# Kernel optimization log

Measured on AMD Instinct MI355X. Metric: run time of the kernel, lower is better.

Reference implementation:

```python
import jax, jax.numpy as jnp
import numpy as np

B, S, E, H, D = 4, 2048, 1024, 8, 128
EPS = 1e-5


def _ln(x, g, b):
    m = jnp.mean(x, axis=-1, keepdims=True)
    v = jnp.mean((x - m) ** 2, axis=-1, keepdims=True)
    return (x - m) * jax.lax.rsqrt(v + EPS) * g + b


def _xavier(k, shape, fan_in, fan_out):
    lim = float(np.sqrt(6.0 / (fan_in + fan_out)))
    return jax.random.uniform(k, shape, jnp.float32, -lim, lim)


def setup_inputs() -> dict:
    key = jax.random.key(0)
    ks = jax.random.split(key, 10)
    return {
        "x": jax.random.normal(ks[0], (B, S, E), jnp.float32),
        # embedding_to_z: Linear(E, H*D); stored as [E, H*D] for x @ W
        "W_ez": _xavier(ks[1], (E, H * D), E, H * D),
        "b_ez": jnp.zeros((H * D,), jnp.float32),
        "U_h": _xavier(ks[2], (H, D, D), D, D),
        "U_z": _xavier(ks[3], (H, D, D), D, D),
        "b_u": jnp.zeros((H, D), jnp.float32),
        "out_shaper": _xavier(ks[4], (H, D, D), D, D),
        # shared per-step state LayerNorm
        "lns_g": jnp.ones((D,), jnp.float32),
        "lns_b": jnp.zeros((D,), jnp.float32),
        # per-head FFN: LayerNorm(D) -> Linear(D,D) -> GELU -> Linear(D,E)
        "ff_ln_g": jnp.ones((H, D), jnp.float32),
        "ff_ln_b": jnp.zeros((H, D), jnp.float32),
        "ff_W1": _xavier(ks[5], (H, D, D), D, D),
        "ff_b1": jnp.zeros((H, D), jnp.float32),
        "ff_W2": _xavier(ks[6], (H, D, E), D, E),
        "ff_b2": jnp.zeros((H, E), jnp.float32),
        # layer_attention_weights: Linear(E, 1)
        "w_att": _xavier(ks[7], (E,), E, 1),
        "b_att": jnp.zeros((), jnp.float32),
        # output LayerNorm
        "lno_g": jnp.ones((E,), jnp.float32),
        "lno_b": jnp.zeros((E,), jnp.float32),
    }


def reference(x, W_ez, b_ez, U_h, U_z, b_u, out_shaper, lns_g, lns_b,
              ff_ln_g, ff_ln_b, ff_W1, ff_b1, ff_W2, ff_b2,
              w_att, b_att, lno_g, lno_b):
    b, s, _ = x.shape
    h, d = U_h.shape[0], U_h.shape[1]
    # z tokens: [B,S,H,D]
    z = jnp.tanh((x @ W_ez + b_ez).reshape(b, s, h, d))
    # torch.einsum('bhd,hdd->bhd') takes the DIAGONAL of the second operand
    uh_diag = jnp.einsum('hii->hi', U_h)          # [H,D]
    uz_diag = jnp.einsum('hii->hi', U_z)          # [H,D]
    os_diag = jnp.einsum('hii->hi', out_shaper)   # [H,D]

    def step(h_prev, z_t):
        # h_prev, z_t: [B,H,D]
        u = jax.nn.sigmoid(h_prev * uh_diag + z_t * uz_diag + b_u)
        h_new = u * h_prev + (1.0 - u) * z_t
        h_new = _ln(h_new, lns_g, lns_b)
        return h_new, h_new

    h0 = jnp.zeros((b, h, d), x.dtype)
    _, states = jax.lax.scan(step, h0, jnp.swapaxes(z, 0, 1))  # [S,B,H,D]
    states = jnp.swapaxes(states, 0, 1)                         # [B,S,H,D]

    shaped = states * os_diag                                   # diag einsum
    hln = _ln(shaped, ff_ln_g, ff_ln_b)                         # per-head LN
    h1 = jax.nn.gelu(jnp.einsum('bshd,hde->bshe', hln, ff_W1) + ff_b1,
                     approximate=False)                         # [B,S,H,D]
    ff_out = jnp.einsum('bshd,hde->bshe', h1, ff_W2) + ff_b2    # [B,S,H,E]

    scores = jax.nn.softmax(jnp.einsum('bshe,e->bsh', ff_out, w_att) + b_att,
                            axis=2)                             # over heads
    weighted = jnp.einsum('bshe,bsh->bse', ff_out, scores)      # [B,S,E]
    return _ln(weighted, lno_g, lno_b)
```

## Files before the change

kernel.cpp:

```cpp
#include <hip/hip_runtime.h>
#include <hip/hip_bf16.h>
#include <math.h>

#define BB 4
#define SS 2048
#define EE 1024
#define HH 8
#define DD 128
#define BSR (BB*SS)
#define HD  (HH*DD)
#define LNEPS 1e-5f
#define LOG2E 1.4426950408889634f

typedef __attribute__((ext_vector_type(8))) short bf16x8;
typedef __attribute__((ext_vector_type(4))) float f32x4;

__device__ __forceinline__ ushort f2bf(float f) {
    union { float f; unsigned u; } c{f};
    unsigned r = c.u + 0x7fff + ((c.u >> 16) & 1);
    return (ushort)(r >> 16);
}
__device__ __forceinline__ float bf2f(ushort b) {
    union { unsigned u; float f; } c{(unsigned)b << 16};
    return c.f;
}

typedef __attribute__((address_space(1))) const unsigned int GUI;
typedef __attribute__((address_space(3))) unsigned int LUI;
__device__ __forceinline__ void gl_lds16(const ushort* g, ushort* l) {
    __builtin_amdgcn_global_load_lds((GUI*)g, (LUI*)l, 16, 0, 0);
}

__global__ __launch_bounds__(256)
void prep_k(const float* __restrict__ W2, const float* __restrict__ w_att,
            const float* __restrict__ b2, const float* __restrict__ b_att,
            const float* __restrict__ Uh, const float* __restrict__ Uz,
            const float* __restrict__ Os,
            float* __restrict__ q, float* __restrict__ c,
            float* __restrict__ uh_d, float* __restrict__ uz_d,
            float* __restrict__ os_d)
{
    const int gid  = blockIdx.x * 256 + threadIdx.x;
    const int wave = gid >> 6, lane = gid & 63;
    if (wave < HD) {
        const float* wp = W2 + (size_t)wave * EE;
        float p = 0.f;
        for (int e = lane; e < EE; e += 64) p = fmaf(wp[e], w_att[e], p);
        #pragma unroll
        for (int off = 32; off > 0; off >>= 1) p += __shfl_xor(p, off, 64);
        if (lane == 0) {
            q[wave] = p;
            const int h = wave >> 7, d = wave & 127;
            uh_d[wave] = Uh[(size_t)h*DD*DD + (size_t)d*DD + d];
            uz_d[wave] = Uz[(size_t)h*DD*DD + (size_t)d*DD + d];
            os_d[wave] = Os[(size_t)h*DD*DD + (size_t)d*DD + d];
        }
    } else if (wave < HD + HH) {
        const int h = wave - HD;
        const float* bp = b2 + (size_t)h * EE;
        float p = 0.f;
        for (int e = lane; e < EE; e += 64) p = fmaf(bp[e], w_att[e], p);
        #pragma unroll
        for (int off = 32; off > 0; off >>= 1) p += __shfl_xor(p, off, 64);
        if (lane == 0) c[h] = p + b_att[0];
    }
}

__global__ __launch_bounds__(256)
void convx2_k(const float* __restrict__ x,
              ushort* __restrict__ hi, ushort* __restrict__ lo)
{
    const size_t idx = ((size_t)blockIdx.x * 256 + threadIdx.x) * 4;
    const float4 v = *(const float4*)(x + idx);
    ushort4 oh, ol;
    oh.x = f2bf(v.x); ol.x = f2bf(v.x - bf2f(oh.x));
    oh.y = f2bf(v.y); ol.y = f2bf(v.y - bf2f(oh.y));
    oh.z = f2bf(v.z); ol.z = f2bf(v.z - bf2f(oh.z));
    oh.w = f2bf(v.w); ol.w = f2bf(v.w - bf2f(oh.w));
    *(ushort4*)(hi + idx) = oh;
    *(ushort4*)(lo + idx) = ol;
}

__global__ __launch_bounds__(256)
void convT2_k(const float* __restrict__ W,
              ushort* __restrict__ Wth, ushort* __restrict__ Wtl)
{
    __shared__ float tile[32][33];
    const int k0 = blockIdx.x * 32, n0 = blockIdx.y * 32;
    const int tx = threadIdx.x & 31, ty = threadIdx.x >> 5;
    #pragma unroll
    for (int i = 0; i < 4; ++i)
        tile[ty + i*8][tx] = W[(size_t)(k0 + ty + i*8) * 1024 + n0 + tx];
    __syncthreads();
    #pragma unroll
    for (int i = 0; i < 4; ++i) {
        const float v = tile[tx][ty + i*8];
        const ushort h = f2bf(v);
        Wth[(size_t)(n0 + ty + i*8) * 1024 + k0 + tx] = h;
        Wtl[(size_t)(n0 + ty + i*8) * 1024 + k0 + tx] = f2bf(v - bf2f(h));
    }
}

__global__ __launch_bounds__(256)
void convT_k(const float* __restrict__ W, ushort* __restrict__ Wt)
{
    __shared__ float tile[32][33];
    const int k0 = blockIdx.x * 32, n0 = blockIdx.y * 32;
    const int tx = threadIdx.x & 31, ty = threadIdx.x >> 5;
    #pragma unroll
    for (int i = 0; i < 4; ++i)
        tile[ty + i*8][tx] = W[(size_t)(k0 + ty + i*8) * 1024 + n0 + tx];
    __syncthreads();
    #pragma unroll
    for (int i = 0; i < 4; ++i)
        Wt[(size_t)(n0 + ty + i*8) * 1024 + k0 + tx] = f2bf(tile[tx][ty + i*8]);
}

__global__ __launch_bounds__(256)
void convTH_k(const float* __restrict__ W, ushort* __restrict__ Wt)
{
    __shared__ float tile[32][33];
    const int hh = blockIdx.z;
    const int k0 = blockIdx.x * 32, n0 = blockIdx.y * 32;
    const int tx = threadIdx.x & 31, ty = threadIdx.x >> 5;
    const float* Wb = W + (size_t)hh * DD * DD;
    ushort*      Wtb = Wt + (size_t)hh * DD * DD;
    #pragma unroll
    for (int i = 0; i < 4; ++i)
        tile[ty + i*8][tx] = Wb[(size_t)(k0 + ty + i*8) * DD + n0 + tx];
    __syncthreads();
    #pragma unroll
    for (int i = 0; i < 4; ++i)
        Wtb[(size_t)(n0 + ty + i*8) * DD + k0 + tx] = f2bf(tile[tx][ty + i*8]);
}

__global__ __launch_bounds__(256)
void gemm_mfma_hp(const ushort* __restrict__ Ah, const ushort* __restrict__ Al,
                  const ushort* __restrict__ Bh, const ushort* __restrict__ Bl,
                  float* __restrict__ C, const float* __restrict__ bias)
{
    __shared__ ushort AsmH[128*32], AsmL[128*32];
    __shared__ ushort BsmH[128*32], BsmL[128*32];
    const int t = threadIdx.x, lane = t & 63, w = t >> 6;
    const int wr = w >> 1, wc = w & 1;
    const int row0 = blockIdx.x * 128, col0 = blockIdx.y * 128;

    const int lr = lane >> 2;
    const int lc = (lane & 3) ^ (lr & 3);
    const size_t aoff0 = (size_t)(row0 +      w*16 + lr) * 1024 + lc*8;
    const size_t aoff1 = (size_t)(row0 + 64 + w*16 + lr) * 1024 + lc*8;
    const size_t boff0 = (size_t)(col0 +      w*16 + lr) * 1024 + lc*8;
    const size_t boff1 = (size_t)(col0 + 64 + w*16 + lr) * 1024 + lc*8;
    ushort* AH0 = AsmH + (     w*16) * 32;  ushort* AH1 = AsmH + (64 + w*16) * 32;
    ushort* AL0 = AsmL + (     w*16) * 32;  ushort* AL1 = AsmL + (64 + w*16) * 32;
    ushort* BH0 = BsmH + (     w*16) * 32;  ushort* BH1 = BsmH + (64 + w*16) * 32;
    ushort* BL0 = BsmL + (     w*16) * 32;  ushort* BL1 = BsmL + (64 + w*16) * 32;

    f32x4 acc[4][4];
    #pragma unroll
    for (int i = 0; i < 4; ++i)
        #pragma unroll
        for (int j = 0; j < 4; ++j) acc[i][j] = (f32x4){0.f,0.f,0.f,0.f};

    const int quad = lane >> 4;
    const int fr   = lane & 15;
    const int fchk = (quad ^ (lane & 3)) * 8;

    for (int k0 = 0; k0 < 1024; k0 += 32) {
        __syncthreads();
        gl_lds16(Ah + aoff0 + k0, AH0);
        gl_lds16(Ah + aoff1 + k0, AH1);
        gl_lds16(Bh + boff0 + k0, BH0);
        gl_lds16(Bh + boff1 + k0, BH1);
        gl_lds16(Al + aoff0 + k0, AL0);
        gl_lds16(Al + aoff1 + k0, AL1);
        gl_lds16(Bl + boff0 + k0, BL0);
        gl_lds16(Bl + boff1 + k0, BL1);
        __syncthreads();

        bf16x8 afh[4], afl[4], bfh[4], bfl[4];
        #pragma unroll
        for (int i = 0; i < 4; ++i) {
            const int ra = (wr*64 + i*16 + fr) * 32 + fchk;
            afh[i] = *(const bf16x8*)(AsmH + ra);
            afl[i] = *(const bf16x8*)(AsmL + ra);
            const int rb = (wc*64 + i*16 + fr) * 32 + fchk;
            bfh[i] = *(const bf16x8*)(BsmH + rb);
            bfl[i] = *(const bf16x8*)(BsmL + rb);
        }
        #pragma unroll
        for (int i = 0; i < 4; ++i)
            #pragma unroll
            for (int j = 0; j < 4; ++j) {
                acc[i][j] = __builtin_amdgcn_mfma_f32_16x16x32_bf16(
                    afh[i], bfl[j], acc[i][j], 0, 0, 0);
                acc[i][j] = __builtin_amdgcn_mfma_f32_16x16x32_bf16(
                    afl[i], bfh[j], acc[i][j], 0, 0, 0);
                acc[i][j] = __builtin_amdgcn_mfma_f32_16x16x32_bf16(
                    afh[i], bfh[j], acc[i][j], 0, 0, 0);
            }
    }

    float colv[4];
    #pragma unroll
    for (int tj = 0; tj < 4; ++tj)
        colv[tj] = bias[col0 + wc*64 + tj*16 + fr];
    #pragma unroll
    for (int ti = 0; ti < 4; ++ti)
        #pragma unroll
        for (int i = 0; i < 4; ++i) {
            const int row = row0 + wr*64 + ti*16 + quad*4 + i;
            #pragma unroll
            for (int tj = 0; tj < 4; ++tj) {
                const int col = col0 + wc*64 + tj*16 + fr;
                C[(size_t)row*1024 + col] = tanhf(acc[ti][tj][i] + colv[tj]);
            }
        }
}

__global__ __launch_bounds__(256)
void gemm_mfma(const ushort* __restrict__ A, const ushort* __restrict__ Bt,
               float* __restrict__ C,
               const float* __restrict__ scores, const float* __restrict__ b2)
{
    __shared__ ushort Asm[128*32];
    __shared__ ushort Bsm[128*32];
    const int t = threadIdx.x, lane = t & 63, w = t >> 6;
    const int wr = w >> 1, wc = w & 1;
    const int row0 = blockIdx.x * 128, col0 = blockIdx.y * 128;

    const int lr = lane >> 2;
    const int lc = (lane & 3) ^ (lr & 3);
    const ushort* Ag0 = A  + (size_t)(row0 +      w*16 + lr) * 1024 + lc*8;
    const ushort* Ag1 = A  + (size_t)(row0 + 64 + w*16 + lr) * 1024 + lc*8;
    const ushort* Bg0 = Bt + (size_t)(col0 +      w*16 + lr) * 1024 + lc*8;
    const ushort* Bg1 = Bt + (size_t)(col0 + 64 + w*16 + lr) * 1024 + lc*8;
    ushort* Al0 = Asm + (     w*16) * 32;
    ushort* Al1 = Asm + (64 + w*16) * 32;
    ushort* Bl0 = Bsm + (     w*16) * 32;
    ushort* Bl1 = Bsm + (64 + w*16) * 32;

    f32x4 acc[4][4];
    #pragma unroll
    for (int i = 0; i < 4; ++i)
        #pragma unroll
        for (int j = 0; j < 4; ++j) acc[i][j] = (f32x4){0.f,0.f,0.f,0.f};

    const int quad = lane >> 4;
    const int fr   = lane & 15;
    const int fchk = (quad ^ (lane & 3)) * 8;

    for (int k0 = 0; k0 < 1024; k0 += 32) {
        __syncthreads();
        gl_lds16(Ag0 + k0, Al0);
        gl_lds16(Ag1 + k0, Al1);
        gl_lds16(Bg0 + k0, Bl0);
        gl_lds16(Bg1 + k0, Bl1);
        __syncthreads();

        bf16x8 af[4], bf[4];
        #pragma unroll
        for (int i = 0; i < 4; ++i) {
            af[i] = *(const bf16x8*)(Asm + (wr*64 + i*16 + fr)*32 + fchk);
            bf[i] = *(const bf16x8*)(Bsm + (wc*64 + i*16 + fr)*32 + fchk);
        }
        #pragma unroll
        for (int i = 0; i < 4; ++i)
            #pragma unroll
            for (int j = 0; j < 4; ++j)
                acc[i][j] = __builtin_amdgcn_mfma_f32_16x16x32_bf16(
                    af[i], bf[j], acc[i][j], 0, 0, 0);
    }

    float b2v[4][HH];
    #pragma unroll
    for (int tj = 0; tj < 4; ++tj) {
        const int col = col0 + wc*64 + tj*16 + fr;
        #pragma unroll
        for (int h = 0; h < HH; ++h) b2v[tj][h] = b2[(size_t)h*EE + col];
    }
    #pragma unroll
    for (int ti = 0; ti < 4; ++ti)
        #pragma unroll
        for (int i = 0; i < 4; ++i) {
            const int row = row0 + wr*64 + ti*16 + quad*4 + i;
            float sc[HH];
            #pragma unroll
            for (int h = 0; h < HH; ++h) sc[h] = scores[row*HH + h];
            #pragma unroll
            for (int tj = 0; tj < 4; ++tj) {
                const int col = col0 + wc*64 + tj*16 + fr;
                float bb = 0.f;
                #pragma unroll
                for (int h = 0; h < HH; ++h) bb = fmaf(sc[h], b2v[tj][h], bb);
                C[(size_t)row*1024 + col] = acc[ti][tj][i] + bb;
            }
        }
}

__global__ __launch_bounds__(256)
void gemm_h1(const ushort* __restrict__ A, const ushort* __restrict__ Bt,
             const float* __restrict__ b1, float* __restrict__ C)
{
    const int hh = blockIdx.z;
    __shared__ ushort Asm[128*32];
    __shared__ ushort Bsm[128*32];
    const int t = threadIdx.x, lane = t & 63, w = t >> 6;
    const int wr = w >> 1, wc = w & 1;
    const int row0 = blockIdx.x * 128;

    const int lr = lane >> 2;
    const int lc = (lane & 3) ^ (lr & 3);
    const ushort* Ag0 = A + (size_t)(row0 +      w*16 + lr) * 1024 + hh*DD + lc*8;
    const ushort* Ag1 = A + (size_t)(row0 + 64 + w*16 + lr) * 1024 + hh*DD + lc*8;
    const ushort* Bg0 = Bt + (size_t)hh*DD*DD + (     w*16 + lr) * DD + lc*8;
    const ushort* Bg1 = Bt + (size_t)hh*DD*DD + (64 + w*16 + lr) * DD + lc*8;
    ushort* Al0 = Asm + (     w*16) * 32;
    ushort* Al1 = Asm + (64 + w*16) * 32;
    ushort* Bl0 = Bsm + (     w*16) * 32;
    ushort* Bl1 = Bsm + (64 + w*16) * 32;

    f32x4 acc[4][4];
    #pragma unroll
    for (int i = 0; i < 4; ++i)
        #pragma unroll
        for (int j = 0; j < 4; ++j) acc[i][j] = (f32x4){0.f,0.f,0.f,0.f};

    const int quad = lane >> 4;
    const int fr   = lane & 15;
    const int fchk = (quad ^ (lane & 3)) * 8;

    for (int k0 = 0; k0 < 128; k0 += 32) {
        __syncthreads();
        gl_lds16(Ag0 + k0, Al0);
        gl_lds16(Ag1 + k0, Al1);
        gl_lds16(Bg0 + k0, Bl0);
        gl_lds16(Bg1 + k0, Bl1);
        __syncthreads();

        bf16x8 af[4], bf[4];
        #pragma unroll
        for (int i = 0; i < 4; ++i) {
            af[i] = *(const bf16x8*)(Asm + (wr*64 + i*16 + fr)*32 + fchk);
            bf[i] = *(const bf16x8*)(Bsm + (wc*64 + i*16 + fr)*32 + fchk);
        }
        #pragma unroll
        for (int i = 0; i < 4; ++i)
            #pragma unroll
            for (int j = 0; j < 4; ++j)
                acc[i][j] = __builtin_amdgcn_mfma_f32_16x16x32_bf16(
                    af[i], bf[j], acc[i][j], 0, 0, 0);
    }

    float colv[4];
    #pragma unroll
    for (int tj = 0; tj < 4; ++tj)
        colv[tj] = b1[hh*DD + wc*64 + tj*16 + fr];
    #pragma unroll
    for (int ti = 0; ti < 4; ++ti)
        #pragma unroll
        for (int i = 0; i < 4; ++i) {
            const int row = row0 + wr*64 + ti*16 + quad*4 + i;
            #pragma unroll
            for (int tj = 0; tj < 4; ++tj) {
                const int col = wc*64 + tj*16 + fr;
                float v = acc[ti][tj][i] + colv[tj];
                v = 0.5f * v * (1.f + erff(v * 0.70710678118654752f));
                C[(size_t)row*1024 + hh*DD + col] = v;
            }
        }
}

__device__ __forceinline__ float dpp_add(float x, const int ctrl) {
    int y;
    switch (ctrl) {
        case 0x111: y = __builtin_amdgcn_update_dpp(0, __float_as_int(x), 0x111, 0xf, 0xf, true); break;
        case 0x112: y = __builtin_amdgcn_update_dpp(0, __float_as_int(x), 0x112, 0xf, 0xf, true); break;
        case 0x114: y = __builtin_amdgcn_update_dpp(0, __float_as_int(x), 0x114, 0xf, 0xf, true); break;
        case 0x118: y = __builtin_amdgcn_update_dpp(0, __float_as_int(x), 0x118, 0xf, 0xf, true); break;
        case 0x142: y = __builtin_amdgcn_update_dpp(0, __float_as_int(x), 0x142, 0xf, 0xf, true); break;
        default:    y = __builtin_amdgcn_update_dpp(0, __float_as_int(x), 0x143, 0xf, 0xf, true); break;
    }
    return x + __int_as_float(y);
}

__device__ __forceinline__ float wave_sum64(float x) {
    x = dpp_add(x, 0x111);
    x = dpp_add(x, 0x112);
    x = dpp_add(x, 0x114);
    x = dpp_add(x, 0x118);
    x = dpp_add(x, 0x142);
    x = dpp_add(x, 0x143);
    return __int_as_float(__builtin_amdgcn_readlane(__float_as_int(x), 63));
}

__global__ __launch_bounds__(64)
void scan_k(const float* __restrict__ z,
            const float* __restrict__ uh_d, const float* __restrict__ uz_d,
            const float* __restrict__ b_u,
            const float* __restrict__ lns_g, const float* __restrict__ lns_b,
            ushort* __restrict__ states)
{
    const int bh = blockIdx.x;
    const int b = bh >> 3, h = bh & 7;
    const int l = threadIdx.x;
    const int d0 = 2*l, d1 = d0 + 1;

    const float uhn0 = -uh_d[h*DD+d0] * LOG2E, uhn1 = -uh_d[h*DD+d1] * LOG2E;
    const float uzn0 = -uz_d[h*DD+d0] * LOG2E, uzn1 = -uz_d[h*DD+d1] * LOG2E;
    const float bun0 = -b_u [h*DD+d0] * LOG2E, bun1 = -b_u [h*DD+d1] * LOG2E;
    const float g0  = lns_g[d0], g1 = lns_g[d1];
    const float be0 = lns_b[d0], be1 = lns_b[d1];
    const float A0 = g0 * uhn0, A1 = g1 * uhn1;
    const float bunB0 = fmaf(be0, uhn0, bun0);
    const float bunB1 = fmaf(be1, uhn1, bun1);

    const float* zp = z + ((size_t)b * SS * HH + h) * DD + d0;
    unsigned* op = (unsigned*)(states + (size_t)b * SS * HD + h * DD) + l;

    const int CH = 8;
    float2 zc[CH], zn[CH];
    float pb0[CH], pb1[CH];
    #pragma unroll
    for (int i = 0; i < CH; ++i) zc[i] = *(const float2*)(zp + (size_t)i*HD);
    #pragma unroll
    for (int i = 0; i < CH; ++i) {
        pb0[i] = fmaf(zc[i].x, uzn0, bunB0);
        pb1[i] = fmaf(zc[i].y, uzn1, bunB1);
    }

    float r_c, wp0, wp1, W0, W1, dv0, dv1;

#define SCAN_STEP(ZX, ZY, PB0v, PB1v, ZNX, ZNY, OFF) do {                    \
        const float t0 = fmaf(r_c, W0, (PB0v));                              \
        const float t1 = fmaf(r_c, W1, (PB1v));                              \
        const float e0 = __builtin_amdgcn_exp2f(t0);                         \
        const float e1 = __builtin_amdgcn_exp2f(t1);                         \
        const float u0 = __builtin_amdgcn_rcpf(1.f + e0);                    \
        const float u1 = __builtin_amdgcn_rcpf(1.f + e1);                    \
        const float hn0 = fmaf(u0, dv0, (ZX));                               \
        const float hn1 = fmaf(u1, dv1, (ZY));                               \
        const float s1 = wave_sum64(hn0 + hn1);                              \
        const float s2 = wave_sum64(fmaf(hn0, hn0, hn1*hn1));                \
        const float m   = s1 * (1.f/128.f);                                  \
        const float var = fmaf(s2, 1.f/128.f, -m*m);                         \
        r_c = __builtin_amdgcn_rsqf(var + LNEPS);                            \
        wp0 = hn0 - m; wp1 = hn1 - m;                                        \
        W0 = wp0 * A0; W1 = wp1 * A1;                                        \
        const float hp0 = fmaf(wp0, r_c * g0, be0);                          \
        const float hp1 = fmaf(wp1, r_c * g1, be1);                          \
        op[(size_t)(OFF) * (HD/2)] =                                         \
            (unsigned)f2bf(hp0) | ((unsigned)f2bf(hp1) << 16);               \
        dv0 = hp0 - (ZNX); dv1 = hp1 - (ZNY);                                \
    } while (0)

    {
        const float z0 = zc[0].x, z1 = zc[0].y;
        const float t0 = fmaf(z0, uzn0, bun0);
        const float t1 = fmaf(z1, uzn1, bun1);
        const float e0 = __builtin_amdgcn_exp2f(t0);
        const float e1 = __builtin_amdgcn_exp2f(t1);
        const float u0 = __builtin_amdgcn_rcpf(1.f + e0);
        const float u1 = __builtin_amdgcn_rcpf(1.f + e1);
        const float hn0 = fmaf(u0, -z0, z0);
        const float hn1 = fmaf(u1, -z1, z1);
        const float s1 = wave_sum64(hn0 + hn1);
        const float s2 = wave_sum64(fmaf(hn0, hn0, hn1*hn1));
        const float m   = s1 * (1.f/128.f);
        const float var = fmaf(s2, 1.f/128.f, -m*m);
        r_c = __builtin_amdgcn_rsqf(var + LNEPS);
        wp0 = hn0 - m; wp1 = hn1 - m;
        W0 = wp0 * A0; W1 = wp1 * A1;
        const float hp0 = fmaf(wp0, r_c * g0, be0);
        const float hp1 = fmaf(wp1, r_c * g1, be1);
        op[0] = (unsigned)f2bf(hp0) | ((unsigned)f2bf(hp1) << 16);
        dv0 = hp0 - zc[1].x; dv1 = hp1 - zc[1].y;
    }

    #pragma unroll
    for (int i = 0; i < CH; ++i)
        zn[i] = *(const float2*)(zp + (size_t)(CH+i)*HD);
    #pragma unroll
    for (int i = 1; i < CH; ++i) {
        const float znx = (i+1 < CH) ? zc[i+1].x : zn[0].x;
        const float zny = (i+1 < CH) ? zc[i+1].y : zn[0].y;
        SCAN_STEP(zc[i].x, zc[i].y, pb0[i], pb1[i], znx, zny, i);
    }
    #pragma unroll
    for (int i = 0; i < CH; ++i) {
        zc[i] = zn[i];
        pb0[i] = fmaf(zn[i].x, uzn0, bunB0);
        pb1[i] = fmaf(zn[i].y, uzn1, bunB1);
    }

    for (int s0 = CH; s0 < SS; s0 += CH) {
        if (s0 + CH < SS) {
            #pragma unroll
            for (int i = 0; i < CH; ++i)
                zn[i] = *(const float2*)(zp + (size_t)(s0+CH+i)*HD);
        } else {
            #pragma unroll
            for (int i = 0; i < CH; ++i) zn[i] = make_float2(0.f, 0.f);
        }
        #pragma unroll
        for (int i = 0; i < CH; ++i) {
            const float znx = (i+1 < CH) ? zc[i+1].x : zn[0].x;
            const float zny = (i+1 < CH) ? zc[i+1].y : zn[0].y;
            SCAN_STEP(zc[i].x, zc[i].y, pb0[i], pb1[i], znx, zny, s0 + i);
        }
        #pragma unroll
        for (int i = 0; i < CH; ++i) {
            zc[i] = zn[i];
            pb0[i] = fmaf(zn[i].x, uzn0, bunB0);
            pb1[i] = fmaf(zn[i].y, uzn1, bunB1);
        }
    }
#undef SCAN_STEP
}

__global__ __launch_bounds__(256)
void headln_k(const unsigned* __restrict__ st, const float* __restrict__ os_d,
              const float* __restrict__ ffg, const float* __restrict__ ffb,
              unsigned* __restrict__ hln)
{
    const int gid  = blockIdx.x * 256 + threadIdx.x;
    const int row  = gid >> 6;
    const int l    = gid & 63;
    const int h = row & 7;
    const int d0 = 2*l, d1 = d0 + 1;
    const unsigned v = st[(size_t)row * 64 + l];
    const float x0 = bf2f((ushort)(v & 0xffff)) * os_d[h*DD + d0];
    const float x1 = bf2f((ushort)(v >> 16))    * os_d[h*DD + d1];
    float s1 = x0 + x1;
    float s2 = fmaf(x0, x0, x1*x1);
    #pragma unroll
    for (int off = 32; off > 0; off >>= 1) {
        s1 += __shfl_xor(s1, off, 64);
        s2 += __shfl_xor(s2, off, 64);
    }
    const float m   = s1 * (1.f/128.f);
    const float var = fmaf(s2, 1.f/128.f, -m*m);
    const float r   = rsqrtf(var + LNEPS);
    const float o0 = fmaf((x0 - m)*r, ffg[h*DD + d0], ffb[h*DD + d0]);
    const float o1 = fmaf((x1 - m)*r, ffg[h*DD + d1], ffb[h*DD + d1]);
    hln[(size_t)row * 64 + l] = (unsigned)f2bf(o0) | ((unsigned)f2bf(o1) << 16);
}

__global__ __launch_bounds__(256)
void logits_k(const float* __restrict__ h1, const float* __restrict__ q,
              const float* __restrict__ c, float* __restrict__ logits)
{
    const int gid  = blockIdx.x * 256 + threadIdx.x;
    const int row  = gid >> 6;
    const int lane = gid & 63;
    const int h = row & 7;
    const float* xp = h1 + (size_t)row * DD;
    float p = fmaf(xp[lane], q[h*DD + lane], xp[lane+64] * q[h*DD + lane + 64]);
    #pragma unroll
    for (int off = 32; off > 0; off >>= 1) p += __shfl_xor(p, off, 64);
    if (lane == 0) logits[row] = p + c[h];
}

__global__ __launch_bounds__(256)
void softscale_k(const float* __restrict__ h1, const float* __restrict__ logits,
                 ushort* __restrict__ gb, float* __restrict__ scores)
{
    const int gid = blockIdx.x * 256 + threadIdx.x;
    const size_t idx = (size_t)gid * 4;
    const int bs = (int)(idx >> 10);
    const int h  = (int)((idx >> 7) & 7);
    float l[8];
    float mx = -1e30f;
    #pragma unroll
    for (int i = 0; i < 8; ++i) { l[i] = logits[bs*8 + i]; mx = fmaxf(mx, l[i]); }
    float den = 0.f;
    #pragma unroll
    for (int i = 0; i < 8; ++i) den += __expf(l[i] - mx);
    const float sc = __expf(l[h] - mx) / den;
    float4 v = *(const float4*)(h1 + idx);
    ushort4 o;
    o.x = f2bf(v.x * sc); o.y = f2bf(v.y * sc);
    o.z = f2bf(v.z * sc); o.w = f2bf(v.w * sc);
    *(ushort4*)(gb + idx) = o;
    if ((idx & 127) == 0) scores[bs*8 + h] = sc;
}

__global__ __launch_bounds__(256)
void finalln_k(const float* __restrict__ w, const float* __restrict__ g,
               const float* __restrict__ b, float* __restrict__ out)
{
    const int row = blockIdx.x;
    const int t = threadIdx.x;
    const float* xp = w + (size_t)row * EE;
    const float4 v = *(const float4*)(xp + t*4);
    float s1 = v.x + v.y + v.z + v.w;
    float s2 = v.x*v.x + v.y*v.y + v.z*v.z + v.w*v.w;
    #pragma unroll
    for (int off = 32; off > 0; off >>= 1) {
        s1 += __shfl_xor(s1, off, 64);
        s2 += __shfl_xor(s2, off, 64);
    }
    __shared__ float r1[4], r2[4];
    if ((t & 63) == 0) { r1[t>>6] = s1; r2[t>>6] = s2; }
    __syncthreads();
    s1 = r1[0] + r1[1] + r1[2] + r1[3];
    s2 = r2[0] + r2[1] + r2[2] + r2[3];
    const float m   = s1 * (1.f/1024.f);
    const float var = fmaf(s2, 1.f/1024.f, -m*m);
    const float r   = rsqrtf(var + LNEPS);
    const float4 gv = *(const float4*)(g + t*4);
    const float4 bv = *(const float4*)(b + t*4);
    float4 o;
    o.x = fmaf((v.x - m)*r, gv.x, bv.x);
    o.y = fmaf((v.y - m)*r, gv.y, bv.y);
    o.z = fmaf((v.z - m)*r, gv.z, bv.z);
    o.w = fmaf((v.w - m)*r, gv.w, bv.w);
    *(float4*)(out + (size_t)row*EE + t*4) = o;
}

extern "C" void kernel_launch(void* const* d_in, const int* in_sizes, int n_in,
                              void* d_out, int out_size, void* d_ws, size_t ws_size,
                              hipStream_t stream)
{
    const float* x       = (const float*)d_in[0];
    const float* W_ez    = (const float*)d_in[1];
    const float* b_ez    = (const float*)d_in[2];
    const float* U_h     = (const float*)d_in[3];
    const float* U_z     = (const float*)d_in[4];
    const float* b_u     = (const float*)d_in[5];
    const float* outsh   = (const float*)d_in[6];
    const float* lns_g   = (const float*)d_in[7];
    const float* lns_b   = (const float*)d_in[8];
    const float* ff_ln_g = (const float*)d_in[9];
    const float* ff_ln_b = (const float*)d_in[10];
    const float* ff_W1   = (const float*)d_in[11];
    const float* ff_b1   = (const float*)d_in[12];
    const float* ff_W2   = (const float*)d_in[13];
    const float* ff_b2   = (const float*)d_in[14];
    const float* w_att   = (const float*)d_in[15];
    const float* b_att   = (const float*)d_in[16];
    const float* lno_g   = (const float*)d_in[17];
    const float* lno_b   = (const float*)d_in[18];
    float* out = (float*)d_out;

    float* ws = (float*)d_ws;
    const size_t NBIG = (size_t)BSR * HD;
    float* bufA = ws;
    float* bufB = ws + NBIG;
    float* bufC = ws + 2*NBIG;
    float* ext  = ws + 3*NBIG;
    ushort* W2t   = (ushort*)ext;
    ushort* W1t   = (ushort*)(ext + 512*1024);
    float* logits = ext + 512*1024 + 64*1024;
    float* scores = logits + BSR*HH;
    float* qv     = scores + BSR*HH;
    float* cv     = qv + HD;
    float* uh_d   = cv + 8;
    float* uz_d   = uh_d + HD;
    float* os_d   = uz_d + HD;
    ushort* xb_hi = (ushort*)bufB;
    ushort* xb_lo = (ushort*)bufB + NBIG;
    ushort* stb   = (ushort*)bufB;
    ushort* hlnb  = (ushort*)bufB + NBIG;
    float*  wsum  = bufB;
    ushort* WezT_hi = (ushort*)bufC;
    ushort* WezT_lo = (ushort*)bufC + 1024*1024;
    float*  h1f   = bufC;
    ushort* gb    = (ushort*)bufA;

    convx2_k<<<(BSR*EE/4)/256, 256, 0, stream>>>(x, xb_hi, xb_lo);
    convT2_k<<<dim3(32, 32), 256, 0, stream>>>(W_ez, WezT_hi, WezT_lo);
    convT_k<<<dim3(32, 32), 256, 0, stream>>>(ff_W2, W2t);
    convTH_k<<<dim3(4, 4, 8), 256, 0, stream>>>(ff_W1, W1t);
    prep_k<<<258, 256, 0, stream>>>(ff_W2, w_att, ff_b2, b_att,
                                    U_h, U_z, outsh, qv, cv, uh_d, uz_d, os_d);
    gemm_mfma_hp<<<dim3(64, 8), 256, 0, stream>>>(
        xb_hi, xb_lo, WezT_hi, WezT_lo, bufA, b_ez);
    scan_k<<<BB*HH, 64, 0, stream>>>(bufA, uh_d, uz_d, b_u, lns_g, lns_b, stb);
    headln_k<<<(BSR*HH*64)/256, 256, 0, stream>>>(
        (const unsigned*)stb, os_d, ff_ln_g, ff_ln_b, (unsigned*)hlnb);
    gemm_h1<<<dim3(64, 1, 8), 256, 0, stream>>>(hlnb, W1t, ff_b1, h1f);
    logits_k<<<(BSR*HH*64)/256, 256, 0, stream>>>(h1f, qv, cv, logits);
    softscale_k<<<(BSR*HD/4)/256, 256, 0, stream>>>(h1f, logits, gb, scores);
    gemm_mfma<<<dim3(64, 8), 256, 0, stream>>>(gb, W2t, wsum, scores, ff_b2);
    finalln_k<<<BSR, 256, 0, stream>>>(wsum, lno_g, lno_b, out);
}
```

Measured before the change: 591.6 us.

## Fuse logits into h1 GEMM epilogue, store h1 as bf16, merge prep kernels

Folds the per-head attention-logit dot product into the h1 GEMM epilogue, using DPP row reductions and a shared-memory combine across the two column waves, which removes the separate logits kernel and one full fp32 read of h1. h1 is now written as bf16, halving its write and the read in softscale. The three weight transpose/convert kernels and the prep kernel are merged into one launch. The scan output packing switches to a perm-based rounding that uses round-half-up instead of round-to-nearest-even, and storing h1 in bf16 adds a small precision loss before the score scaling.

```diff
diff --git a/kernel.cpp b/kernel.cpp
--- a/kernel.cpp
+++ b/kernel.cpp
@@ -31,39 +31,27 @@
     __builtin_amdgcn_global_load_lds((GUI*)g, (LUI*)l, 16, 0, 0);
 }
 
-__global__ __launch_bounds__(256)
-void prep_k(const float* __restrict__ W2, const float* __restrict__ w_att,
-            const float* __restrict__ b2, const float* __restrict__ b_att,
-            const float* __restrict__ Uh, const float* __restrict__ Uz,
-            const float* __restrict__ Os,
-            float* __restrict__ q, float* __restrict__ c,
-            float* __restrict__ uh_d, float* __restrict__ uz_d,
-            float* __restrict__ os_d)
-{
-    const int gid  = blockIdx.x * 256 + threadIdx.x;
-    const int wave = gid >> 6, lane = gid & 63;
-    if (wave < HD) {
-        const float* wp = W2 + (size_t)wave * EE;
-        float p = 0.f;
-        for (int e = lane; e < EE; e += 64) p = fmaf(wp[e], w_att[e], p);
-        #pragma unroll
-        for (int off = 32; off > 0; off >>= 1) p += __shfl_xor(p, off, 64);
-        if (lane == 0) {
-            q[wave] = p;
-            const int h = wave >> 7, d = wave & 127;
-            uh_d[wave] = Uh[(size_t)h*DD*DD + (size_t)d*DD + d];
-            uz_d[wave] = Uz[(size_t)h*DD*DD + (size_t)d*DD + d];
-            os_d[wave] = Os[(size_t)h*DD*DD + (size_t)d*DD + d];
-        }
-    } else if (wave < HD + HH) {
-        const int h = wave - HD;
-        const float* bp = b2 + (size_t)h * EE;
-        float p = 0.f;
-        for (int e = lane; e < EE; e += 64) p = fmaf(bp[e], w_att[e], p);
-        #pragma unroll
-        for (int off = 32; off > 0; off >>= 1) p += __shfl_xor(p, off, 64);
-        if (lane == 0) c[h] = p + b_att[0];
-    }
+__device__ __forceinline__ float dpp_add(float x, const int ctrl) {
+    int y;
+    switch (ctrl) {
+        case 0x111: y = __builtin_amdgcn_update_dpp(0, __float_as_int(x), 0x111, 0xf, 0xf, true); break;
+        case 0x112: y = __builtin_amdgcn_update_dpp(0, __float_as_int(x), 0x112, 0xf, 0xf, true); break;
+        case 0x114: y = __builtin_amdgcn_update_dpp(0, __float_as_int(x), 0x114, 0xf, 0xf, true); break;
+        case 0x118: y = __builtin_amdgcn_update_dpp(0, __float_as_int(x), 0x118, 0xf, 0xf, true); break;
+        case 0x142: y = __builtin_amdgcn_update_dpp(0, __float_as_int(x), 0x142, 0xf, 0xf, true); break;
+        default:    y = __builtin_amdgcn_update_dpp(0, __float_as_int(x), 0x143, 0xf, 0xf, true); break;
+    }
+    return x + __int_as_float(y);
+}
+
+__device__ __forceinline__ float wave_sum64(float x) {
+    x = dpp_add(x, 0x111);
+    x = dpp_add(x, 0x112);
+    x = dpp_add(x, 0x114);
+    x = dpp_add(x, 0x118);
+    x = dpp_add(x, 0x142);
+    x = dpp_add(x, 0x143);
+    return __int_as_float(__builtin_amdgcn_readlane(__float_as_int(x), 63));
 }
 
 __global__ __launch_bounds__(256)
@@ -82,56 +70,83 @@
 }
 
 __global__ __launch_bounds__(256)
-void convT2_k(const float* __restrict__ W,
-              ushort* __restrict__ Wth, ushort* __restrict__ Wtl)
+void prepall_k(const float* __restrict__ W_ez,
+               ushort* __restrict__ Wth, ushort* __restrict__ Wtl,
+               const float* __restrict__ W2, ushort* __restrict__ W2t,
+               const float* __restrict__ W1, ushort* __restrict__ W1t,
+               const float* __restrict__ w_att, const float* __restrict__ b2,
+               const float* __restrict__ b_att,
+               const float* __restrict__ Uh, const float* __restrict__ Uz,
+               const float* __restrict__ Os,
+               float* __restrict__ q, float* __restrict__ c,
+               float* __restrict__ uh_d, float* __restrict__ uz_d,
+               float* __restrict__ os_d)
 {
     __shared__ float tile[32][33];
-    const int k0 = blockIdx.x * 32, n0 = blockIdx.y * 32;
+    const int blk = blockIdx.x;
     const int tx = threadIdx.x & 31, ty = threadIdx.x >> 5;
-    #pragma unroll
-    for (int i = 0; i < 4; ++i)
-        tile[ty + i*8][tx] = W[(size_t)(k0 + ty + i*8) * 1024 + n0 + tx];
-    __syncthreads();
-    #pragma unroll
-    for (int i = 0; i < 4; ++i) {
-        const float v = tile[tx][ty + i*8];
-        const ushort h = f2bf(v);
-        Wth[(size_t)(n0 + ty + i*8) * 1024 + k0 + tx] = h;
-        Wtl[(size_t)(n0 + ty + i*8) * 1024 + k0 + tx] = f2bf(v - bf2f(h));
-    }
-}
-
-__global__ __launch_bounds__(256)
-void convT_k(const float* __restrict__ W, ushort* __restrict__ Wt)
-{
-    __shared__ float tile[32][33];
-    const int k0 = blockIdx.x * 32, n0 = blockIdx.y * 32;
-    const int tx = threadIdx.x & 31, ty = threadIdx.x >> 5;
-    #pragma unroll
-    for (int i = 0; i < 4; ++i)
-        tile[ty + i*8][tx] = W[(size_t)(k0 + ty + i*8) * 1024 + n0 + tx];
-    __syncthreads();
-    #pragma unroll
-    for (int i = 0; i < 4; ++i)
-        Wt[(size_t)(n0 + ty + i*8) * 1024 + k0 + tx] = f2bf(tile[tx][ty + i*8]);
-}
-
-__global__ __launch_bounds__(256)
-void convTH_k(const float* __restrict__ W, ushort* __restrict__ Wt)
-{
-    __shared__ float tile[32][33];
-    const int hh = blockIdx.z;
-    const int k0 = blockIdx.x * 32, n0 = blockIdx.y * 32;
-    const int tx = threadIdx.x & 31, ty = threadIdx.x >> 5;
-    const float* Wb = W + (size_t)hh * DD * DD;
-    ushort*      Wtb = Wt + (size_t)hh * DD * DD;
-    #pragma unroll
-    for (int i = 0; i < 4; ++i)
-        tile[ty + i*8][tx] = Wb[(size_t)(k0 + ty + i*8) * DD + n0 + tx];
-    __syncthreads();
-    #pragma unroll
-    for (int i = 0; i < 4; ++i)
-        Wtb[(size_t)(n0 + ty + i*8) * DD + k0 + tx] = f2bf(tile[tx][ty + i*8]);
+    if (blk < 1024) {
+        const int k0 = (blk >> 5) * 32, n0 = (blk & 31) * 32;
+        #pragma unroll
+        for (int i = 0; i < 4; ++i)
+            tile[ty + i*8][tx] = W_ez[(size_t)(k0 + ty + i*8) * 1024 + n0 + tx];
+        __syncthreads();
+        #pragma unroll
+        for (int i = 0; i < 4; ++i) {
+            const float v = tile[tx][ty + i*8];
+            const ushort h = f2bf(v);
+            Wth[(size_t)(n0 + ty + i*8) * 1024 + k0 + tx] = h;
+            Wtl[(size_t)(n0 + ty + i*8) * 1024 + k0 + tx] = f2bf(v - bf2f(h));
+        }
+    } else if (blk < 2048) {
+        const int b2i = blk - 1024;
+        const int k0 = (b2i >> 5) * 32, n0 = (b2i & 31) * 32;
+        #pragma unroll
+        for (int i = 0; i < 4; ++i)
+            tile[ty + i*8][tx] = W2[(size_t)(k0 + ty + i*8) * 1024 + n0 + tx];
+        __syncthreads();
+        #pragma unroll
+        for (int i = 0; i < 4; ++i)
+            W2t[(size_t)(n0 + ty + i*8) * 1024 + k0 + tx] = f2bf(tile[tx][ty + i*8]);
+    } else if (blk < 2176) {
+        const int idx = blk - 2048;
+        const int hh = idx >> 4;
+        const int k0 = (idx & 3) * 32, n0 = ((idx >> 2) & 3) * 32;
+        const float* Wb = W1 + (size_t)hh * DD * DD;
+        ushort*      Wtb = W1t + (size_t)hh * DD * DD;
+        #pragma unroll
+        for (int i = 0; i < 4; ++i)
+            tile[ty + i*8][tx] = Wb[(size_t)(k0 + ty + i*8) * DD + n0 + tx];
+        __syncthreads();
+        #pragma unroll
+        for (int i = 0; i < 4; ++i)
+            Wtb[(size_t)(n0 + ty + i*8) * DD + k0 + tx] = f2bf(tile[tx][ty + i*8]);
+    } else {
+        const int gid  = (blk - 2176) * 256 + threadIdx.x;
+        const int wave = gid >> 6, lane = gid & 63;
+        if (wave < HD) {
+            const float* wp = W2 + (size_t)wave * EE;
+            float p = 0.f;
+            for (int e = lane; e < EE; e += 64) p = fmaf(wp[e], w_att[e], p);
+            #pragma unroll
+            for (int off = 32; off > 0; off >>= 1) p += __shfl_xor(p, off, 64);
+            if (lane == 0) {
+                q[wave] = p;
+                const int h = wave >> 7, d = wave & 127;
+                uh_d[wave] = Uh[(size_t)h*DD*DD + (size_t)d*DD + d];
+                uz_d[wave] = Uz[(size_t)h*DD*DD + (size_t)d*DD + d];
+                os_d[wave] = Os[(size_t)h*DD*DD + (size_t)d*DD + d];
+            }
+        } else if (wave < HD + HH) {
+            const int h = wave - HD;
+            const float* bp = b2 + (size_t)h * EE;
+            float p = 0.f;
+            for (int e = lane; e < EE; e += 64) p = fmaf(bp[e], w_att[e], p);
+            #pragma unroll
+            for (int off = 32; off > 0; off >>= 1) p += __shfl_xor(p, off, 64);
+            if (lane == 0) c[h] = p + b_att[0];
+        }
+    }
 }
 
 __global__ __launch_bounds__(256)
@@ -300,11 +315,14 @@
 
 __global__ __launch_bounds__(256)
 void gemm_h1(const ushort* __restrict__ A, const ushort* __restrict__ Bt,
-             const float* __restrict__ b1, float* __restrict__ C)
+             const float* __restrict__ b1,
+             const float* __restrict__ qv, const float* __restrict__ cv,
+             ushort* __restrict__ h1b, float* __restrict__ logits)
 {
     const int hh = blockIdx.z;
     __shared__ ushort Asm[128*32];
     __shared__ ushort Bsm[128*32];
+    __shared__ float lpart[128][2];
     const int t = threadIdx.x, lane = t & 63, w = t >> 6;
     const int wr = w >> 1, wc = w & 1;
     const int row0 = blockIdx.x * 128;
@@ -352,46 +370,37 @@
                     af[i], bf[j], acc[i][j], 0, 0, 0);
     }
 
-    float colv[4];
-    #pragma unroll
-    for (int tj = 0; tj < 4; ++tj)
-        colv[tj] = b1[hh*DD + wc*64 + tj*16 + fr];
+    float colv[4], qh[4];
+    #pragma unroll
+    for (int tj = 0; tj < 4; ++tj) {
+        const int col = wc*64 + tj*16 + fr;
+        colv[tj] = b1[hh*DD + col];
+        qh[tj]   = qv[hh*DD + col];
+    }
     #pragma unroll
     for (int ti = 0; ti < 4; ++ti)
         #pragma unroll
         for (int i = 0; i < 4; ++i) {
             const int row = row0 + wr*64 + ti*16 + quad*4 + i;
+            float p = 0.f;
             #pragma unroll
             for (int tj = 0; tj < 4; ++tj) {
                 const int col = wc*64 + tj*16 + fr;
                 float v = acc[ti][tj][i] + colv[tj];
                 v = 0.5f * v * (1.f + erff(v * 0.70710678118654752f));
-                C[(size_t)row*1024 + hh*DD + col] = v;
+                h1b[(size_t)row*1024 + hh*DD + col] = f2bf(v);
+                p = fmaf(v, qh[tj], p);
             }
-        }
-}
-
-__device__ __forceinline__ float dpp_add(float x, const int ctrl) {
-    int y;
-    switch (ctrl) {
-        case 0x111: y = __builtin_amdgcn_update_dpp(0, __float_as_int(x), 0x111, 0xf, 0xf, true); break;
-        case 0x112: y = __builtin_amdgcn_update_dpp(0, __float_as_int(x), 0x112, 0xf, 0xf, true); break;
-        case 0x114: y = __builtin_amdgcn_update_dpp(0, __float_as_int(x), 0x114, 0xf, 0xf, true); break;
-        case 0x118: y = __builtin_amdgcn_update_dpp(0, __float_as_int(x), 0x118, 0xf, 0xf, true); break;
-        case 0x142: y = __builtin_amdgcn_update_dpp(0, __float_as_int(x), 0x142, 0xf, 0xf, true); break;
-        default:    y = __builtin_amdgcn_update_dpp(0, __float_as_int(x), 0x143, 0xf, 0xf, true); break;
-    }
-    return x + __int_as_float(y);
-}
-
-__device__ __forceinline__ float wave_sum64(float x) {
-    x = dpp_add(x, 0x111);
-    x = dpp_add(x, 0x112);
-    x = dpp_add(x, 0x114);
-    x = dpp_add(x, 0x118);
-    x = dpp_add(x, 0x142);
-    x = dpp_add(x, 0x143);
-    return __int_as_float(__builtin_amdgcn_readlane(__float_as_int(x), 63));
+            p = dpp_add(p, 0x111);
+            p = dpp_add(p, 0x112);
+            p = dpp_add(p, 0x114);
+            p = dpp_add(p, 0x118);
+            if (fr == 15)
+                lpart[wr*64 + ti*16 + quad*4 + i][wc] = p;
+        }
+    __syncthreads();
+    if (t < 128)
+        logits[(size_t)(row0 + t)*HH + hh] = lpart[t][0] + lpart[t][1] + cv[hh];
 }
 
 __global__ __launch_bounds__(64)
@@ -430,6 +439,13 @@
     }
 
     float r_c, wp0, wp1, W0, W1, dv0, dv1;
+
+#define PACK_STORE(HP0, HP1, OFF) do {                                       \
+        const unsigned pu0 = __float_as_uint(HP0) + 0x8000u;                 \
+        const unsigned pu1 = __float_as_uint(HP1) + 0x8000u;                 \
+        op[(size_t)(OFF) * (HD/2)] =                                         \
+            __builtin_amdgcn_perm(pu1, pu0, 0x07060302u);                    \
+    } while (0)
 
 #define SCAN_STEP(ZX, ZY, PB0v, PB1v, ZNX, ZNY, OFF) do {                    \
         const float t0 = fmaf(r_c, W0, (PB0v));                              \
@@ -449,8 +465,7 @@
         W0 = wp0 * A0; W1 = wp1 * A1;                                        \
         const float hp0 = fmaf(wp0, r_c * g0, be0);                          \
         const float hp1 = fmaf(wp1, r_c * g1, be1);                          \
-        op[(size_t)(OFF) * (HD/2)] =                                         \
-            (unsigned)f2bf(hp0) | ((unsigned)f2bf(hp1) << 16);               \
+        PACK_STORE(hp0, hp1, OFF);                                           \
         dv0 = hp0 - (ZNX); dv1 = hp1 - (ZNY);                                \
     } while (0)
 
@@ -473,7 +488,7 @@
         W0 = wp0 * A0; W1 = wp1 * A1;
         const float hp0 = fmaf(wp0, r_c * g0, be0);
         const float hp1 = fmaf(wp1, r_c * g1, be1);
-        op[0] = (unsigned)f2bf(hp0) | ((unsigned)f2bf(hp1) << 16);
+        PACK_STORE(hp0, hp1, 0);
         dv0 = hp0 - zc[1].x; dv1 = hp1 - zc[1].y;
     }
 
@@ -516,6 +531,7 @@
         }
     }
 #undef SCAN_STEP
+#undef PACK_STORE
 }
 
 __global__ __launch_bounds__(256)
@@ -547,22 +563,7 @@
 }
 
 __global__ __launch_bounds__(256)
-void logits_k(const float* __restrict__ h1, const float* __restrict__ q,
-              const float* __restrict__ c, float* __restrict__ logits)
-{
-    const int gid  = blockIdx.x * 256 + threadIdx.x;
-    const int row  = gid >> 6;
-    const int lane = gid & 63;
-    const int h = row & 7;
-    const float* xp = h1 + (size_t)row * DD;
-    float p = fmaf(xp[lane], q[h*DD + lane], xp[lane+64] * q[h*DD + lane + 64]);
-    #pragma unroll
-    for (int off = 32; off > 0; off >>= 1) p += __shfl_xor(p, off, 64);
-    if (lane == 0) logits[row] = p + c[h];
-}
-
-__global__ __launch_bounds__(256)
-void softscale_k(const float* __restrict__ h1, const float* __restrict__ logits,
+void softscale_k(const ushort* __restrict__ h1b, const float* __restrict__ logits,
                  ushort* __restrict__ gb, float* __restrict__ scores)
 {
     const int gid = blockIdx.x * 256 + threadIdx.x;
@@ -577,10 +578,10 @@
     #pragma unroll
     for (int i = 0; i < 8; ++i) den += __expf(l[i] - mx);
     const float sc = __expf(l[h] - mx) / den;
-    float4 v = *(const float4*)(h1 + idx);
+    const ushort4 v = *(const ushort4*)(h1b + idx);
     ushort4 o;
-    o.x = f2bf(v.x * sc); o.y = f2bf(v.y * sc);
-    o.z = f2bf(v.z * sc); o.w = f2bf(v.w * sc);
+    o.x = f2bf(bf2f(v.x) * sc); o.y = f2bf(bf2f(v.y) * sc);
+    o.z = f2bf(bf2f(v.z) * sc); o.w = f2bf(bf2f(v.w) * sc);
     *(ushort4*)(gb + idx) = o;
     if ((idx & 127) == 0) scores[bs*8 + h] = sc;
 }
@@ -665,23 +666,23 @@
     float*  wsum  = bufB;
     ushort* WezT_hi = (ushort*)bufC;
     ushort* WezT_lo = (ushort*)bufC + 1024*1024;
-    float*  h1f   = bufC;
+    ushort* h1b   = (ushort*)bufC;
     ushort* gb    = (ushort*)bufA;
 
     convx2_k<<<(BSR*EE/4)/256, 256, 0, stream>>>(x, xb_hi, xb_lo);
-    convT2_k<<<dim3(32, 32), 256, 0, stream>>>(W_ez, WezT_hi, WezT_lo);
-    convT_k<<<dim3(32, 32), 256, 0, stream>>>(ff_W2, W2t);
-    convTH_k<<<dim3(4, 4, 8), 256, 0, stream>>>(ff_W1, W1t);
-    prep_k<<<258, 256, 0, stream>>>(ff_W2, w_att, ff_b2, b_att,
-                                    U_h, U_z, outsh, qv, cv, uh_d, uz_d, os_d);
+    prepall_k<<<2434, 256, 0, stream>>>(W_ez, WezT_hi, WezT_lo,
+                                        ff_W2, W2t, ff_W1, W1t,
+                                        w_att, ff_b2, b_att,
+                                        U_h, U_z, outsh,
+                                        qv, cv, uh_d, uz_d, os_d);
     gemm_mfma_hp<<<dim3(64, 8), 256, 0, stream>>>(
         xb_hi, xb_lo, WezT_hi, WezT_lo, bufA, b_ez);
     scan_k<<<BB*HH, 64, 0, stream>>>(bufA, uh_d, uz_d, b_u, lns_g, lns_b, stb);
     headln_k<<<(BSR*HH*64)/256, 256, 0, stream>>>(
         (const unsigned*)stb, os_d, ff_ln_g, ff_ln_b, (unsigned*)hlnb);
-    gemm_h1<<<dim3(64, 1, 8), 256, 0, stream>>>(hlnb, W1t, ff_b1, h1f);
-    logits_k<<<(BSR*HH*64)/256, 256, 0, stream>>>(h1f, qv, cv, logits);
-    softscale_k<<<(BSR*HD/4)/256, 256, 0, stream>>>(h1f, logits, gb, scores);
+    gemm_h1<<<dim3(64, 1, 8), 256, 0, stream>>>(hlnb, W1t, ff_b1, qv, cv,
+                                                h1b, logits);
+    softscale_k<<<(BSR*HD/4)/256, 256, 0, stream>>>(h1b, logits, gb, scores);
     gemm_mfma<<<dim3(64, 8), 256, 0, stream>>>(gb, W2t, wsum, scores, ff_b2);
     finalln_k<<<BSR, 256, 0, stream>>>(wsum, lno_g, lno_b, out);
 }
```

New measurement: 566.9 us. -4.2%, faster.
